# Performance work log

Hardware: AMD Instinct MI355X
Metric: run time of the kernel (lower is better)

## Reference

```python
import jax, jax.numpy as jnp
import numpy as np

B, N_LINES, C_FEAT = 16, 200, 64
H_IMG = W_IMG = 256
NUM_BINS = 32
LINE_LENGTH = 64
LINE_LENGTH_MINUS_1_HALF = (LINE_LENGTH - 1) / 2.0
MIN_CONTINUOUS_DISTANCE = 6.0
FUNCTION_AMPLITUDE = 0.43
FUNCTION_SLOPE = 0.5
EPS = 1e-05


def _unnorm(coord, size):
    # torch grid_sample align_corners=False: pixel = ((g + 1) * size - 1) / 2
    return ((coord + 1.0) * size - 1.0) * 0.5


def _gather2d(img, yi, xi, valid):
    # img (B,C,H,W); yi/xi (B,N,L) int32 in-range; zeros padding via valid mask
    g = jax.vmap(lambda im, yy, xx: im[:, yy, xx])(img, yi, xi)  # (B,C,N,L)
    return g * valid[:, None].astype(img.dtype)


def grid_sample_nearest(img, grid):
    _, _, H, W = img.shape
    x = _unnorm(grid[..., 0], W)
    y = _unnorm(grid[..., 1], H)
    xi = jnp.round(x).astype(jnp.int32)
    yi = jnp.round(y).astype(jnp.int32)
    valid = (xi >= 0) & (xi < W) & (yi >= 0) & (yi < H)
    return _gather2d(img, jnp.clip(yi, 0, H - 1), jnp.clip(xi, 0, W - 1), valid)


def grid_sample_bilinear(img, grid):
    _, _, H, W = img.shape
    x = _unnorm(grid[..., 0], W)
    y = _unnorm(grid[..., 1], H)
    x0 = jnp.floor(x)
    y0 = jnp.floor(y)
    wx1 = x - x0
    wy1 = y - y0
    x0i = x0.astype(jnp.int32)
    y0i = y0.astype(jnp.int32)
    out = jnp.zeros(img.shape[:2] + grid.shape[1:3], dtype=img.dtype)
    for dx, wx in ((0, 1.0 - wx1), (1, wx1)):
        for dy, wy in ((0, 1.0 - wy1), (1, wy1)):
            xi = x0i + dx
            yi = y0i + dy
            valid = (xi >= 0) & (xi < W) & (yi >= 0) & (yi < H)
            g = _gather2d(img, jnp.clip(yi, 0, H - 1), jnp.clip(xi, 0, W - 1), valid)
            out = out + g * (wx * wy)[:, None]
    return out


def setup_inputs() -> dict:
    key = jax.random.key(0)
    k = jax.random.split(key, 6)
    image = jax.random.uniform(k[0], (B, 3, H_IMG, W_IMG), dtype=jnp.float32)
    feature = jax.random.normal(k[1], (B, C_FEAT, H_IMG, W_IMG), dtype=jnp.float32)
    pose = jnp.concatenate([
        jnp.tile(jnp.eye(3, dtype=jnp.float32).reshape(1, 9), (B, 1)),
        jnp.tile(jnp.array([[0.0, 0.0, 0.5]], dtype=jnp.float32), (B, 1)),
    ], axis=-1)  # identity rotation, 0.5m in front of camera
    camera_data = jnp.tile(
        jnp.array([[float(W_IMG), float(H_IMG), 300.0, 300.0, 128.0, 128.0]], dtype=jnp.float32),
        (B, 1))  # [w, h, fx, fy, cx, cy]
    centers = jax.random.normal(k[2], (B, N_LINES, 3), dtype=jnp.float32) * 0.05
    normals = jax.random.normal(k[3], (B, N_LINES, 3), dtype=jnp.float32)
    normals = normals / jnp.linalg.norm(normals, axis=-1, keepdims=True)
    dists = jnp.full((B, N_LINES, 2), 0.02, dtype=jnp.float32)
    template_view = jnp.concatenate([centers, normals, dists], axis=-1)  # (B,N,8)
    fore_hist = jax.random.uniform(k[4], (B, NUM_BINS ** 3), dtype=jnp.float32)
    back_hist = jax.random.uniform(k[5], (B, NUM_BINS ** 3), dtype=jnp.float32)
    return {"image": image, "feature": feature,
            "init_body2view_pose_data": pose, "camera_data": camera_data,
            "template_view": template_view, "fore_hist": fore_hist,
            "back_hist": back_hist}


def reference(image, feature, init_body2view_pose_data, camera_data, template_view,
              fore_hist, back_hist):
    R = init_body2view_pose_data[:, :9].reshape(-1, 3, 3)
    t = init_body2view_pose_data[:, 9:]
    centers_in_body = template_view[..., :3]
    normals_in_body = template_view[..., 3:6]
    fg_dist = template_view[..., 6]
    bg_dist = template_view[..., 7]

    # transform / rotate (p3d @ R^T + t)
    centers_in_view = jnp.einsum('bnj,bij->bni', centers_in_body, R) + t[:, None]
    normals_in_view = jnp.einsum('bnj,bij->bni', normals_in_body, R)

    # project_p3d
    z = centers_in_view[..., 2]
    valid1 = z > 1e-4
    p2d = centers_in_view[..., :2] / jnp.maximum(z, 1e-4)[..., None]
    f = camera_data[:, 2:4]
    c = camera_data[:, 4:6]
    size = camera_data[:, :2]
    centers_in_image = p2d * f[:, None] + c[:, None]
    in_b = (centers_in_image >= 0) & (centers_in_image <= size[:, None] - 1)
    centers_valid = valid1 & in_b[..., 0] & in_b[..., 1]

    n2 = normals_in_view[..., :2]
    normals_in_image = n2 / jnp.maximum(jnp.linalg.norm(n2, axis=-1, keepdims=True), 1e-12)

    cur_fg = fg_dist * f[:, 0:1] / z
    cur_bg = bg_dist * f[:, 0:1] / z
    continuous_distance = jnp.minimum(cur_fg, cur_bg)  # fscale = 1 in forward
    valid_data_line = (continuous_distance >= MIN_CONTINUOUS_DISTANCE) & centers_valid

    width, height = feature.shape[2], feature.shape[3]

    # build search-line sample points: (B,N,L,2)
    step = jnp.arange(LINE_LENGTH, dtype=centers_in_image.dtype) - LINE_LENGTH_MINUS_1_HALF
    points = centers_in_image[:, :, None, :] + step[None, None, :, None] * normals_in_image[:, :, None, :]

    def _in_bounds(p):
        return (p[..., 0] >= 0) & (p[..., 0] < width) & (p[..., 1] >= 0) & (p[..., 1] < height)

    valid_data_line = valid_data_line & _in_bounds(points[:, :, 0]) & _in_bounds(points[:, :, -1])

    grid = jnp.stack([points[..., 0] / width * 2 - 1,
                      points[..., 1] / height * 2 - 1], axis=-1)

    # nearest sample of RGB image -> histogram fg/bg probability lookup
    lines_image = grid_sample_nearest(image, grid)  # (B,3,N,L)
    bins = jnp.clip((lines_image * NUM_BINS).astype(jnp.int32), 0, NUM_BINS - 1)
    hist_idx = (bins[:, 0] * NUM_BINS + bins[:, 1]) * NUM_BINS + bins[:, 2]  # (B,N,L)
    pf = jax.vmap(lambda h, i: h[i])(fore_hist, hist_idx)
    pb = jax.vmap(lambda h, i: h[i])(back_hist, hist_idx)
    zero_idx = (pf < EPS) & (pb < EPS)
    pf = jnp.where(zero_idx, EPS, pf)
    pb = jnp.where(zero_idx, EPS, pb)
    psum = pf + pb
    pf = pf / psum  # lines_image_pf_segments (second eps/normalize pass is a no-op)
    pb = pb / psum  # lines_image_pb_segments

    lines_feature = grid_sample_bilinear(feature, grid)  # (B,C,N,L)
    lines_amplitude = jnp.full(pf.shape[:2], FUNCTION_AMPLITUDE, dtype=feature.dtype)
    lines_slope = jnp.full(pf.shape[:2], FUNCTION_SLOPE, dtype=feature.dtype)

    return (normals_in_image, centers_in_image, centers_in_body, pf, pb,
            valid_data_line, lines_amplitude, lines_slope, lines_feature)
```

## Files before the change

### kernel.cpp

```cpp
#include <hip/hip_runtime.h>

#define BN     16
#define NLINES 200
#define CFEAT  64
#define HIMG   256
#define WIMG   256
#define LLEN   64
#define NBINS  32

#define O_NORM   0
#define O_CIMG   6400
#define O_CBODY  12800
#define O_PF     22400
#define O_PB     227200
#define O_VALID  432000
#define O_AMP    435200
#define O_SLOPE  438400
#define O_FEAT   441600

#define NPTS (BN*NLINES*LLEN)

struct LineGeom {
  float cix, ciy;
  float nix, niy;
  float cb0, cb1, cb2;
  bool  vdl;
};

__device__ __forceinline__ LineGeom compute_line(
    const float* __restrict__ pose, const float* __restrict__ cam,
    const float* __restrict__ tv, int b, int n)
{
  const float* P = pose + b*12;
  float R00=P[0],R01=P[1],R02=P[2];
  float R10=P[3],R11=P[4],R12=P[5];
  float R20=P[6],R21=P[7],R22=P[8];
  float t0=P[9], t1=P[10], t2=P[11];
  const float* C = cam + b*6;
  float sx=C[0], sy=C[1], fx=C[2], fy=C[3];
  float cx=C[4], cy=C[5];
  const float* T = tv + (b*NLINES + n)*8;
  float cb0=T[0], cb1=T[1], cb2=T[2];
  float nb0=T[3], nb1=T[4], nb2=T[5];
  float fg=T[6],  bg=T[7];

  float cv0 = R00*cb0 + R01*cb1 + R02*cb2 + t0;
  float cv1 = R10*cb0 + R11*cb1 + R12*cb2 + t1;
  float cv2 = R20*cb0 + R21*cb1 + R22*cb2 + t2;
  float nv0 = R00*nb0 + R01*nb1 + R02*nb2;
  float nv1 = R10*nb0 + R11*nb1 + R12*nb2;

  float z  = cv2;
  float zc = fmaxf(z, 1e-4f);
  float cix = (cv0/zc)*fx + cx;
  float ciy = (cv1/zc)*fy + cy;
  bool inb = (cix >= 0.f) && (cix <= sx - 1.f) && (ciy >= 0.f) && (ciy <= sy - 1.f);
  bool centers_valid = (z > 1e-4f) && inb;

  float nrm = fmaxf(sqrtf(nv0*nv0 + nv1*nv1), 1e-12f);
  float nix = nv0/nrm, niy = nv1/nrm;

  float contd = fminf(fg*fx/z, bg*fx/z);
  bool vdl = (contd >= 6.0f) && centers_valid;

  float px0 = cix + (-31.5f)*nix, py0 = ciy + (-31.5f)*niy;
  float px1 = cix + ( 31.5f)*nix, py1 = ciy + ( 31.5f)*niy;
  vdl = vdl && (px0 >= 0.f) && (px0 < 256.f) && (py0 >= 0.f) && (py0 < 256.f)
            && (px1 >= 0.f) && (px1 < 256.f) && (py1 >= 0.f) && (py1 < 256.f);

  LineGeom g;
  g.cix = cix; g.ciy = ciy; g.nix = nix; g.niy = niy;
  g.cb0 = cb0; g.cb1 = cb1; g.cb2 = cb2; g.vdl = vdl;
  return g;
}

__device__ __forceinline__ void point_xy(const LineGeom& g, int i, float& x, float& y)
{
  float s  = (float)i - 31.5f;
  float px = g.cix + s*g.nix;
  float py = g.ciy + s*g.niy;
  float gx = px/256.0f*2.0f - 1.0f;
  float gy = py/256.0f*2.0f - 1.0f;
  x = ((gx + 1.0f)*256.0f - 1.0f)*0.5f;
  y = ((gy + 1.0f)*256.0f - 1.0f)*0.5f;
}

template <bool PRE>
__device__ __forceinline__ void points_body(const float* __restrict__ image,
                                            const float* __restrict__ pose,
                                            const float* __restrict__ cam,
                                            const float* __restrict__ tv,
                                            const float* __restrict__ fore,
                                            const float* __restrict__ back,
                                            float* __restrict__ out,
                                            int4*  __restrict__ offs,
                                            float4* __restrict__ wts)
{
  int tid = blockIdx.x*256 + threadIdx.x;
  int i  = tid & 63;
  int ln = tid >> 6;
  int n  = ln % NLINES;
  int b  = ln / NLINES;

  LineGeom g = compute_line(pose, cam, tv, b, n);

  float x, y;
  point_xy(g, i, x, y);

  float xr = rintf(x), yr = rintf(y);
  int xi = (int)xr, yi = (int)yr;
  bool v = (xi >= 0) && (xi < WIMG) && (yi >= 0) && (yi < HIMG);
  int xc = min(max(xi, 0), WIMG-1), yc = min(max(yi, 0), HIMG-1);
  const float* ib = image + (size_t)b*3*HIMG*WIMG + yc*WIMG + xc;
  float r0 = v ? ib[0]           : 0.f;
  float r1 = v ? ib[HIMG*WIMG]   : 0.f;
  float r2 = v ? ib[2*HIMG*WIMG] : 0.f;

  int b0 = min(max((int)(r0*32.f), 0), NBINS-1);
  int b1 = min(max((int)(r1*32.f), 0), NBINS-1);
  int b2 = min(max((int)(r2*32.f), 0), NBINS-1);
  int hidx = (b0*NBINS + b1)*NBINS + b2;

  float pf = fore[b*NBINS*NBINS*NBINS + hidx];
  float pb = back[b*NBINS*NBINS*NBINS + hidx];
  if (pf < 1e-5f && pb < 1e-5f) { pf = 1e-5f; pb = 1e-5f; }
  float ps = pf + pb;
  pf /= ps; pb /= ps;

  out[O_PF + ln*LLEN + i] = pf;
  out[O_PB + ln*LLEN + i] = pb;

  if (i == 0) {
    out[O_NORM  + ln*2 + 0] = g.nix;
    out[O_NORM  + ln*2 + 1] = g.niy;
    out[O_CIMG  + ln*2 + 0] = g.cix;
    out[O_CIMG  + ln*2 + 1] = g.ciy;
    out[O_CBODY + ln*3 + 0] = g.cb0;
    out[O_CBODY + ln*3 + 1] = g.cb1;
    out[O_CBODY + ln*3 + 2] = g.cb2;
    out[O_VALID + ln] = g.vdl ? 1.0f : 0.0f;
    out[O_AMP   + ln] = 0.43f;
    out[O_SLOPE + ln] = 0.5f;
  }

  if (PRE) {
    float x0f = floorf(x), y0f = floorf(y);
    float wx1 = x - x0f, wy1 = y - y0f;
    float wx0 = 1.0f - wx1, wy0 = 1.0f - wy1;
    int x0 = (int)x0f, y0 = (int)y0f;
    int x1 = x0 + 1,  y1 = y0 + 1;
    bool vx0 = (x0 >= 0) && (x0 < WIMG);
    bool vx1 = (x1 >= 0) && (x1 < WIMG);
    bool vy0 = (y0 >= 0) && (y0 < HIMG);
    bool vy1 = (y1 >= 0) && (y1 < HIMG);
    float4 w;
    w.x = wx0*wy0 * ((vx0 && vy0) ? 1.f : 0.f);
    w.y = wx1*wy0 * ((vx1 && vy0) ? 1.f : 0.f);
    w.z = wx0*wy1 * ((vx0 && vy1) ? 1.f : 0.f);
    w.w = wx1*wy1 * ((vx1 && vy1) ? 1.f : 0.f);
    int xc0 = min(max(x0,0), WIMG-1), xc1 = min(max(x1,0), WIMG-1);
    int yc0 = min(max(y0,0), HIMG-1), yc1 = min(max(y1,0), HIMG-1);
    int4 o;
    o.x = yc0*WIMG + xc0;
    o.y = yc0*WIMG + xc1;
    o.z = yc1*WIMG + xc0;
    o.w = yc1*WIMG + xc1;
    offs[tid] = o;
    wts[tid]  = w;
  }
}

__global__ __launch_bounds__(256)
void contour_points_pre_kernel(const float* __restrict__ image,
                               const float* __restrict__ pose,
                               const float* __restrict__ cam,
                               const float* __restrict__ tv,
                               const float* __restrict__ fore,
                               const float* __restrict__ back,
                               float* __restrict__ out,
                               int4*  __restrict__ offs,
                               float4* __restrict__ wts)
{
  points_body<true>(image, pose, cam, tv, fore, back, out, offs, wts);
}

__global__ __launch_bounds__(256)
void contour_points_kernel(const float* __restrict__ image,
                           const float* __restrict__ pose,
                           const float* __restrict__ cam,
                           const float* __restrict__ tv,
                           const float* __restrict__ fore,
                           const float* __restrict__ back,
                           float* __restrict__ out)
{
  points_body<false>(image, pose, cam, tv, fore, back, out, nullptr, nullptr);
}

__global__ __launch_bounds__(256)
void contour_gather_kernel(const float* __restrict__ feature,
                           const int4*  __restrict__ offs,
                           const float4* __restrict__ wts,
                           float* __restrict__ out)
{
  int tid  = blockIdx.x*256 + threadIdx.x;
  int i    = tid & 63;
  int rest = tid >> 6;
  int n    = rest % NLINES;
  int bc   = rest / NLINES;
  int b    = bc >> 6;

  int p = (b*NLINES + n)*LLEN + i;
  int4   o = offs[p];
  float4 w = wts[p];

  const float* fp = feature + ((size_t)bc << 16);
  float val = w.x*fp[o.x] + w.y*fp[o.y] + w.z*fp[o.z] + w.w*fp[o.w];
  out[O_FEAT + tid] = val;
}

__global__ __launch_bounds__(256)
void contour_feature_kernel(const float* __restrict__ feature,
                            const float* __restrict__ pose,
                            const float* __restrict__ cam,
                            const float* __restrict__ tv,
                            float* __restrict__ out)
{
  int ln = blockIdx.x;
  int n  = ln % NLINES;
  int b  = ln / NLINES;
  int t  = threadIdx.x;
  int i  = t & 63;
  int w  = t >> 6;

  LineGeom g = compute_line(pose, cam, tv, b, n);
  float x, y;
  point_xy(g, i, x, y);

  float x0f = floorf(x), y0f = floorf(y);
  float wx1 = x - x0f, wy1 = y - y0f;
  float wx0 = 1.0f - wx1, wy0 = 1.0f - wy1;
  int x0 = (int)x0f, y0 = (int)y0f;
  int x1 = x0 + 1,  y1 = y0 + 1;
  bool vx0 = (x0 >= 0) && (x0 < WIMG);
  bool vx1 = (x1 >= 0) && (x1 < WIMG);
  bool vy0 = (y0 >= 0) && (y0 < HIMG);
  bool vy1 = (y1 >= 0) && (y1 < HIMG);
  float w00 = wx0*wy0 * ((vx0 && vy0) ? 1.f : 0.f);
  float w10 = wx1*wy0 * ((vx1 && vy0) ? 1.f : 0.f);
  float w01 = wx0*wy1 * ((vx0 && vy1) ? 1.f : 0.f);
  float w11 = wx1*wy1 * ((vx1 && vy1) ? 1.f : 0.f);
  int xc0 = min(max(x0,0), WIMG-1), xc1 = min(max(x1,0), WIMG-1);
  int yc0 = min(max(y0,0), HIMG-1), yc1 = min(max(y1,0), HIMG-1);
  int off00 = yc0*WIMG + xc0;
  int off10 = yc0*WIMG + xc1;
  int off01 = yc1*WIMG + xc0;
  int off11 = yc1*WIMG + xc1;

  const float* fbase = feature + (size_t)b*CFEAT*HIMG*WIMG;
  size_t obase = (size_t)O_FEAT + (((size_t)b*CFEAT)*NLINES + n)*LLEN + i;

  #pragma unroll
  for (int k = 0; k < 16; ++k) {
    int c = w*16 + k;
    const float* fc = fbase + (size_t)c*HIMG*WIMG;
    float val = w00*fc[off00] + w10*fc[off10]
              + w01*fc[off01] + w11*fc[off11];
    out[obase + (size_t)c*NLINES*LLEN] = val;
  }
}

extern "C" void kernel_launch(void* const* d_in, const int* in_sizes, int n_in,
                              void* d_out, int out_size, void* d_ws, size_t ws_size,
                              hipStream_t stream) {
  const float* image   = (const float*)d_in[0];
  const float* feature = (const float*)d_in[1];
  const float* pose    = (const float*)d_in[2];
  const float* cam     = (const float*)d_in[3];
  const float* tv      = (const float*)d_in[4];
  const float* fore    = (const float*)d_in[5];
  const float* back    = (const float*)d_in[6];
  float* out = (float*)d_out;

  const size_t need = (size_t)NPTS * (sizeof(int4) + sizeof(float4));
  if (ws_size >= need) {
    int4*   offs = (int4*)d_ws;
    float4* wts  = (float4*)((char*)d_ws + (size_t)NPTS*sizeof(int4));
    contour_points_pre_kernel<<<NPTS/256, 256, 0, stream>>>(
        image, pose, cam, tv, fore, back, out, offs, wts);
    contour_gather_kernel<<<(BN*CFEAT*NLINES*LLEN)/256, 256, 0, stream>>>(
        feature, offs, wts, out);
  } else {
    contour_points_kernel<<<NPTS/256, 256, 0, stream>>>(
        image, pose, cam, tv, fore, back, out);
    contour_feature_kernel<<<BN*NLINES, 256, 0, stream>>>(
        feature, pose, cam, tv, out);
  }
}
```

Before: 439.1 us.

## Gather two feature channels per thread with XCD-aware block mapping

The gather kernel now has each thread handle two adjacent feature channels, so every precomputed offset/weight record is loaded once and used for two channels. Block indices are remapped so consecutive channel groups land on the same XCD (bid & 7), which is meant to keep a feature plane's cache lines within one XCD's L2. The grid is halved. This cuts offset/weight traffic and should improve L2 locality, at the cost of fewer threads and more outstanding loads per thread.

```diff
diff --git a/kernel.cpp b/kernel.cpp
--- a/kernel.cpp
+++ b/kernel.cpp
@@ -197,25 +197,40 @@
 }
 
 __global__ __launch_bounds__(256)
-void contour_gather_kernel(const float* __restrict__ feature,
-                           const int4*  __restrict__ offs,
-                           const float4* __restrict__ wts,
-                           float* __restrict__ out)
-{
-  int tid  = blockIdx.x*256 + threadIdx.x;
-  int i    = tid & 63;
-  int rest = tid >> 6;
-  int n    = rest % NLINES;
-  int bc   = rest / NLINES;
-  int b    = bc >> 6;
+void contour_gather2_kernel(const float* __restrict__ feature,
+                            const int4*  __restrict__ offs,
+                            const float4* __restrict__ wts,
+                            float* __restrict__ out)
+{
+  int bid = blockIdx.x;
+  int xcd = bid & 7;
+  int q   = bid >> 3;
+  int j   = q % 50;
+  int ug  = q / 50;
+  int u   = ug*8 + xcd;
+  int b   = u >> 5;
+  int c2  = u & 31;
+  int c   = c2 << 1;
+
+  int idx = j*256 + (int)threadIdx.x;
+  int n   = idx >> 6;
+  int i   = idx & 63;
 
   int p = (b*NLINES + n)*LLEN + i;
   int4   o = offs[p];
   float4 w = wts[p];
 
-  const float* fp = feature + ((size_t)bc << 16);
-  float val = w.x*fp[o.x] + w.y*fp[o.y] + w.z*fp[o.z] + w.w*fp[o.w];
-  out[O_FEAT + tid] = val;
+  const float* f0 = feature + ((size_t)(b*CFEAT + c) << 16);
+  const float* f1 = f0 + (1 << 16);
+
+  float a00 = f0[o.x], a01 = f0[o.y], a02 = f0[o.z], a03 = f0[o.w];
+  float a10 = f1[o.x], a11 = f1[o.y], a12 = f1[o.z], a13 = f1[o.w];
+  float v0 = w.x*a00 + w.y*a01 + w.z*a02 + w.w*a03;
+  float v1 = w.x*a10 + w.y*a11 + w.z*a12 + w.w*a13;
+
+  size_t ob = (size_t)O_FEAT + (((size_t)(b*CFEAT + c))*NLINES + n)*LLEN + i;
+  out[ob] = v0;
+  out[ob + (size_t)(NLINES*LLEN)] = v1;
 }
 
 __global__ __launch_bounds__(256)
@@ -287,7 +302,7 @@
     float4* wts  = (float4*)((char*)d_ws + (size_t)NPTS*sizeof(int4));
     contour_points_pre_kernel<<<NPTS/256, 256, 0, stream>>>(
         image, pose, cam, tv, fore, back, out, offs, wts);
-    contour_gather_kernel<<<(BN*CFEAT*NLINES*LLEN)/256, 256, 0, stream>>>(
+    contour_gather2_kernel<<<(BN*CFEAT*NLINES*LLEN)/(2*256), 256, 0, stream>>>(
         feature, offs, wts, out);
   } else {
     contour_points_kernel<<<NPTS/256, 256, 0, stream>>>(
```

After: 428.3 us. 1.03x faster.
